# Kernel optimization log

Measured on AMD Instinct MI355X. Metric: run time of the kernel, lower is better.

Reference implementation:

```python
import jax, jax.numpy as jnp
import numpy as np

B, S, E, D, H, DH, FF, L = 8, 1024, 256, 1024, 16, 64, 4096, 12
TIME_DIM = 4096
MAX_PERIOD = 10000.0


def setup_inputs() -> dict:
    key = jax.random.key(0)
    ks = jax.random.split(key, 12)
    n = lambda k, shp: jax.random.normal(k, shp, dtype=jnp.float32) * 0.02
    return dict(
        inputs=jax.random.normal(ks[0], (B, S, 2 * E), dtype=jnp.float32),
        time=jax.random.uniform(ks[1], (B,), dtype=jnp.float32),
        in_W=n(ks[2], (2 * E, D)), in_b=jnp.zeros((D,), jnp.float32),
        out_W=n(ks[3], (D, E)), out_b=jnp.zeros((E,), jnp.float32),
        t_W1=n(ks[4], (D, TIME_DIM)), t_b1=jnp.zeros((TIME_DIM,), jnp.float32),
        t_W2=n(ks[5], (TIME_DIM, D)), t_b2=jnp.zeros((D,), jnp.float32),
        ln_scale=jnp.ones((L, D), jnp.float32),
        ln_bias=jnp.zeros((L, D), jnp.float32),
        proj_W=n(ks[6], (L, D, 3 * H * DH + 2 * FF)),
        attn_W=n(ks[7], (L, H * DH, D)),
        ff_W=n(ks[8], (L, FF, D)),
    )


def _layernorm(x, g, b):
    m = jnp.mean(x, axis=-1, keepdims=True)
    v = jnp.mean(jnp.square(x - m), axis=-1, keepdims=True)
    return (x - m) * jax.lax.rsqrt(v + 1e-5) * g + b


def reference(inputs, time, in_W, in_b, out_W, out_b, t_W1, t_b1, t_W2, t_b2,
              ln_scale, ln_bias, proj_W, attn_W, ff_W):
    # --- time embedding (SinusoidalTimeEmbedding -> Linear -> GELU -> Linear -> GELU) ---
    half = D // 2
    inv_ts = jnp.exp(jnp.arange(half, dtype=jnp.float32) * (-np.log(MAX_PERIOD) / (half - 1.0)))
    ts = time[:, None] * inv_ts[None, :]                      # [B, D/2]
    temb = jnp.concatenate([jnp.sin(ts), jnp.cos(ts)], -1)     # [B, D]
    temb = jax.nn.gelu(temb @ t_W1 + t_b1, approximate=False)
    temb = jax.nn.gelu(temb @ t_W2 + t_b2, approximate=False)  # [B, D]
    # --- fixed position embedding ---
    inv_freq = 1.0 / (MAX_PERIOD ** (jnp.arange(0, D, 2, dtype=jnp.float32) / D))
    sinu = jnp.arange(S, dtype=jnp.float32)[:, None] * inv_freq[None, :]  # [S, D/2]
    pos = jnp.concatenate([jnp.sin(sinu), jnp.cos(sinu)], -1)             # [S, D]
    # --- input projection + additive embeddings ---
    h = inputs @ in_W + in_b + pos[None] + temb[:, None, :]    # [B, S, D]
    scale = 1.0 / np.sqrt(DH)

    def block(h, params):
        g, bln, Wp, Wa, Wf = params
        u = _layernorm(h, g, bln)
        proj = u @ Wp                                          # [B, S, 3*H*DH + 2*FF]
        q, k, v, ff, gate = jnp.split(
            proj, [H * DH, 2 * H * DH, 3 * H * DH, 3 * H * DH + FF], axis=-1)
        q = q.reshape(B, S, H, DH).transpose(0, 2, 1, 3)       # [B, H, S, DH]
        k = k.reshape(B, S, H, DH).transpose(0, 2, 1, 3)
        v = v.reshape(B, S, H, DH).transpose(0, 2, 1, 3)
        score = jnp.einsum('bhsd,bhtd->bhst', q, k) * scale
        w = jax.nn.softmax(score, axis=-1)
        a = jnp.einsum('bhst,bhtd->bhsd', w, v)
        a = a.transpose(0, 2, 1, 3).reshape(B, S, H * DH)      # merge heads
        attn_out = a @ Wa
        ff_out = (ff * jax.nn.gelu(gate, approximate=True)) @ Wf  # tanh GELU per torch
        return h + attn_out + ff_out, None

    h, _ = jax.lax.scan(block, h, (ln_scale, ln_bias, proj_W, attn_W, ff_W))
    return h @ out_W + out_b
```

## Files before the change

kernel.cpp:

```cpp
#include <hip/hip_runtime.h>
#include <hip/hip_bf16.h>
#include <math.h>

static constexpr int B_ = 8, S_ = 1024, E_ = 256, D_ = 1024, H_ = 16, DH_ = 64,
                     FF_ = 4096, L_ = 12, TDIM_ = 4096;
static constexpr int BS_ = B_ * S_;
static constexpr int PROJN_ = 3 * H_ * DH_ + 2 * FF_;
static constexpr int PROJK_ = 2 * H_ * DH_;
static constexpr int AOW_ = H_ * DH_ + FF_;

typedef __attribute__((ext_vector_type(8))) short bf16x8;
typedef __attribute__((ext_vector_type(4))) short bf16x4;
typedef __attribute__((ext_vector_type(4))) float f32x4;

__device__ __forceinline__ float b2f(short b) {
    return __uint_as_float(((unsigned)(unsigned short)b) << 16);
}
__device__ __forceinline__ short f2b(float f) {
    __hip_bfloat16 h = __float2bfloat16(f);
    return *reinterpret_cast<short*>(&h);
}
__device__ __forceinline__ float gelu_exact(float x) {
    return 0.5f * x * (1.f + erff(x * 0.70710678118654752440f));
}
__device__ __forceinline__ float gelu_tanh(float x) {
    float u2 = 1.59576912160573070f * (x + 0.044715f * x * x * x);
    return x / (1.f + __expf(-u2));
}

#define GLOAD16(g, l)                                                     \
    __builtin_amdgcn_global_load_lds(                                     \
        (const __attribute__((address_space(1))) void*)(g),               \
        (__attribute__((address_space(3))) void*)(l), 16, 0, 0)

__global__ void temb0_kernel(const float* __restrict__ time, float* __restrict__ temb0) {
    int b = blockIdx.x;
    int i = threadIdx.x;
    float inv_ts = expf((float)i * (-logf(10000.f) / 511.f));
    float ts = time[b] * inv_ts;
    temb0[b * D_ + i] = sinf(ts);
    temb0[b * D_ + 512 + i] = cosf(ts);
}

__global__ void pos_kernel(float* __restrict__ pos) {
    int s = blockIdx.x;
    int j = threadIdx.x;
    float inv_freq = expf((float)j * (-logf(10000.f) / 512.f));
    float arg = (float)s * inv_freq;
    pos[s * D_ + j] = sinf(arg);
    pos[s * D_ + 512 + j] = cosf(arg);
}

__global__ void tmlp_kernel(const float* __restrict__ A, const float* __restrict__ Bw,
                            const float* __restrict__ bias, float* __restrict__ C,
                            int K, int N) {
    __shared__ float Ast[8][256];
    __shared__ float red2[16][16][9];
    int t = threadIdx.x;
    int col = t & 15, ks = t >> 4;
    int n = blockIdx.x * 16 + col;
    float acc[8];
#pragma unroll
    for (int b = 0; b < 8; ++b) acc[b] = 0.f;
    for (int c0 = 0; c0 < K; c0 += 256) {
#pragma unroll
        for (int i = 0; i < 8; ++i) {
            int idx = t + i * 256;
            Ast[idx >> 8][idx & 255] = A[(idx >> 8) * K + c0 + (idx & 255)];
        }
        __syncthreads();
#pragma unroll
        for (int i = 0; i < 16; ++i) {
            int k = ks * 16 + i;
            float w = Bw[(size_t)(c0 + k) * N + n];
#pragma unroll
            for (int b = 0; b < 8; ++b) acc[b] = fmaf(Ast[b][k], w, acc[b]);
        }
        __syncthreads();
    }
#pragma unroll
    for (int b = 0; b < 8; ++b) red2[ks][col][b] = acc[b];
    __syncthreads();
    if (t < 128) {
        int c2 = t >> 3, b = t & 7;
        float s = 0.f;
#pragma unroll
        for (int k2 = 0; k2 < 16; ++k2) s += red2[k2][c2][b];
        int nn = blockIdx.x * 16 + c2;
        C[(size_t)b * N + nn] = gelu_exact(s + bias[nn]);
    }
}

__global__ void f2b4_kernel(const float* __restrict__ in, __hip_bfloat16* __restrict__ out) {
    size_t i = ((size_t)blockIdx.x * 256 + threadIdx.x) * 4;
    float4 v = *reinterpret_cast<const float4*>(in + i);
    bf16x4 o;
    o[0] = f2b(v.x); o[1] = f2b(v.y); o[2] = f2b(v.z); o[3] = f2b(v.w);
    *reinterpret_cast<bf16x4*>(reinterpret_cast<short*>(out) + i) = o;
}

__device__ __forceinline__ void convT_body(const float* __restrict__ W,
                                           __hip_bfloat16* __restrict__ Wt,
                                           int K, int N, int outStride, int colOff,
                                           int perm, int bx, int by) {
    __shared__ float tile[64][65];
    int t = threadIdx.x;
    int n0 = bx * 64, k0 = by * 64;
#pragma unroll
    for (int i = 0; i < 4; ++i) {
        int idx = t + i * 256;
        int row = idx >> 4, c4 = (idx & 15) * 4;
        float4 v = *reinterpret_cast<const float4*>(W + (size_t)(k0 + row) * N + n0 + c4);
        tile[row][c4 + 0] = v.x; tile[row][c4 + 1] = v.y;
        tile[row][c4 + 2] = v.z; tile[row][c4 + 3] = v.w;
    }
    __syncthreads();
#pragma unroll
    for (int i = 0; i < 4; ++i) {
        int idx = t + i * 256;
        int n = idx >> 4, k4 = (idx & 15) * 4;
        int ng = n0 + n;
        size_t orow;
        if (perm) {
            if (ng < 3072) orow = ng;
            else if (ng < 7168) { int j = ng - 3072; orow = 3072 + (j >> 7) * 256 + (j & 127); }
            else { int j = ng - 7168; orow = 3072 + (j >> 7) * 256 + 128 + (j & 127); }
        } else {
            orow = ng;
        }
        bf16x4 o;
#pragma unroll
        for (int j = 0; j < 4; ++j) o[j] = f2b(tile[k4 + j][n]);
        *reinterpret_cast<bf16x4*>(reinterpret_cast<short*>(Wt) + orow * outStride + colOff + k0 + k4) = o;
    }
}

__global__ void convT_kernel(const float* __restrict__ W, __hip_bfloat16* __restrict__ Wt,
                             int K, int N, int outStride, int colOff) {
    convT_body(W, Wt, K, N, outStride, colOff, 0, blockIdx.x, blockIdx.y);
}

__global__ void convT3_kernel(const float* __restrict__ Wp, const float* __restrict__ Wa,
                              const float* __restrict__ Wf, __hip_bfloat16* __restrict__ Wpt,
                              __hip_bfloat16* __restrict__ Waft) {
    int bid = blockIdx.x;
    if (bid < 2816) {
        convT_body(Wp, Wpt, D_, PROJN_, D_, 0, 1, bid % 176, bid / 176);
    } else if (bid < 3072) {
        int i2 = bid - 2816;
        convT_body(Wa, Waft, D_, D_, AOW_, 0, 0, i2 & 15, i2 >> 4);
    } else {
        int i2 = bid - 3072;
        convT_body(Wf, Waft, FF_, D_, AOW_, D_, 0, i2 & 15, i2 >> 4);
    }
}

__global__ void ln_kernel(const float* __restrict__ h, const float* __restrict__ g,
                          const float* __restrict__ bb, __hip_bfloat16* __restrict__ u) {
    int row = blockIdx.x;
    int t = threadIdx.x;
    const float4 v = reinterpret_cast<const float4*>(h + (size_t)row * D_)[t];
    __shared__ float red[8];
    float s = v.x + v.y + v.z + v.w;
    for (int m8 = 1; m8 < 64; m8 <<= 1) s += __shfl_xor(s, m8, 64);
    if ((t & 63) == 0) red[t >> 6] = s;
    __syncthreads();
    float mean = (red[0] + red[1] + red[2] + red[3]) * (1.f / 1024.f);
    float dx = v.x - mean, dy = v.y - mean, dz = v.z - mean, dw = v.w - mean;
    float sq = dx * dx + dy * dy + dz * dz + dw * dw;
    for (int m8 = 1; m8 < 64; m8 <<= 1) sq += __shfl_xor(sq, m8, 64);
    if ((t & 63) == 0) red[4 + (t >> 6)] = sq;
    __syncthreads();
    float var = (red[4] + red[5] + red[6] + red[7]) * (1.f / 1024.f);
    float inv = rsqrtf(var + 1e-5f);
    int c = t * 4;
    bf16x4 o;
    o[0] = f2b(dx * inv * g[c + 0] + bb[c + 0]);
    o[1] = f2b(dy * inv * g[c + 1] + bb[c + 1]);
    o[2] = f2b(dz * inv * g[c + 2] + bb[c + 2]);
    o[3] = f2b(dw * inv * g[c + 3] + bb[c + 3]);
    *reinterpret_cast<bf16x4*>(reinterpret_cast<short*>(u) + (size_t)row * D_ + c) = o;
}

template <int MODE, int BIAS, int ADDPE>
__global__ __launch_bounds__(256) void mfma_gemm(
    const __hip_bfloat16* __restrict__ A, const __hip_bfloat16* __restrict__ Bt,
    const float* __restrict__ bias, float* __restrict__ Cf,
    __hip_bfloat16* __restrict__ Cb, const float* __restrict__ pe_pos,
    const float* __restrict__ pe_temb, int M, int N, int K) {
    __shared__ __align__(16) char As[128 * 64];
    __shared__ __align__(16) char Bs[128 * 64];
    int t = threadIdx.x;
    int lane = t & 63, wid = t >> 6;
    int m0 = blockIdx.y * 128, n0 = blockIdx.x * 128;
    size_t rowb = (size_t)K * 2;
    int srow = wid * 32 + (lane >> 2);
    int scol = (lane & 3) * 16;
    const char* ag0 = (const char*)A + (size_t)(m0 + srow) * rowb + scol;
    const char* ag1 = (const char*)A + (size_t)(m0 + srow + 16) * rowb + scol;
    const char* bg0 = (const char*)Bt + (size_t)(n0 + srow) * rowb + scol;
    const char* bg1 = (const char*)Bt + (size_t)(n0 + srow + 16) * rowb + scol;
    int lb0 = wid * 32 * 64;
    int lb1 = lb0 + 16 * 64;
    int wr = (wid >> 1) * 64, wc = (wid & 1) * 64;
    int lr = lane & 15;
    int a_base = (wr + lr) * 64 + (lane >> 4) * 16;
    int b_base = (wc + lr) * 64 + (lane >> 4) * 16;
    f32x4 acc[4][4] = {};
    int nkt = K >> 5;
    for (int kt = 0; kt < nkt; ++kt) {
        GLOAD16(ag0, As + lb0);
        GLOAD16(ag1, As + lb1);
        GLOAD16(bg0, Bs + lb0);
        GLOAD16(bg1, Bs + lb1);
        ag0 += 64; ag1 += 64; bg0 += 64; bg1 += 64;
        __syncthreads();
        bf16x8 af[4], bf[4];
#pragma unroll
        for (int f = 0; f < 4; ++f) {
            af[f] = *reinterpret_cast<const bf16x8*>(As + a_base + f * 1024);
            bf[f] = *reinterpret_cast<const bf16x8*>(Bs + b_base + f * 1024);
        }
        __builtin_amdgcn_s_setprio(1);
#pragma unroll
        for (int i = 0; i < 4; ++i)
#pragma unroll
            for (int j = 0; j < 4; ++j)
                acc[i][j] = __builtin_amdgcn_mfma_f32_16x16x32_bf16(af[i], bf[j], acc[i][j], 0, 0, 0);
        __builtin_amdgcn_s_setprio(0);
        __syncthreads();
    }
    int crow0 = m0 + wr + (lane >> 4) * 4;
    int ccol0 = n0 + wc + lr;
#pragma unroll
    for (int i = 0; i < 4; ++i) {
#pragma unroll
        for (int j = 0; j < 4; ++j) {
            int col = ccol0 + j * 16;
            float bv = BIAS ? bias[col] : 0.f;
            f32x4 v = acc[i][j];
#pragma unroll
            for (int r = 0; r < 4; ++r) {
                int row = crow0 + i * 16 + r;
                size_t o = (size_t)row * N + col;
                float val = v[r] + bv;
                if (ADDPE)
                    val += pe_pos[(size_t)(row & 1023) * D_ + col] +
                           pe_temb[(size_t)(row >> 10) * D_ + col];
                if (MODE == 0) Cf[o] = val;
                else if (MODE == 1) Cb[o] = __float2bfloat16(val);
                else Cf[o] += val;
            }
        }
    }
}

template <int MODE>
__global__ __launch_bounds__(512, 2) void gemm256(
    const __hip_bfloat16* __restrict__ A, const __hip_bfloat16* __restrict__ Bt,
    float* __restrict__ Cf, __hip_bfloat16* __restrict__ Cb,
    __hip_bfloat16* __restrict__ Fb, __hip_bfloat16* __restrict__ Vt,
    int M, int N, int K) {
    __shared__ __align__(16) char lds[131072];
    const int t = threadIdx.x;
    const int lane = t & 63, wid = t >> 6;
    const int lr = lane & 15, g = lane >> 4;
    const int wr = wid >> 2, wc = wid & 3;
    const int nbx = gridDim.x;
    const int nwg = nbx * gridDim.y;
    const int bid = blockIdx.y * nbx + blockIdx.x;
    const int swz = (bid & 7) * (nwg >> 3) + (bid >> 3);
    const int bx = swz % nbx, by = swz / nbx;
    const int m0 = by * 256, n0 = bx * 256;
    const size_t rowb = (size_t)K * 2;
    const int NT = K >> 6;
    const int srow = lane >> 2;
    const int scol = ((lane & 3) ^ (((lane >> 5) & 1) << 1)) * 16;
    const int ga = (g ^ (((lr >> 3) & 1) << 1)) * 16;
    const int arow = wr * 16 + lr;
    const int brow = wc * 16 + lr;
    const char* Ab = (const char*)A;
    const char* Bb = (const char*)Bt;

    auto stage = [&](int mat, int kt, int hh) {
        if (kt >= NT) return;
        int rbase = (mat ? n0 : m0) + hh * 128 + wid * 16 + srow;
        const char* src = (mat ? Bb : Ab) + (size_t)rbase * rowb + (size_t)kt * 128 + scol;
        char* dst = lds + mat * 65536 + (kt & 1) * 32768 + (hh * 128 + wid * 16) * 64;
        GLOAD16(src, dst);
        GLOAD16(src + 64, dst + 16384);
    };

    f32x4 acc[8][4] = {};
    bf16x8 af[4][2], bfr[4][2];

    stage(0, 0, 0); stage(0, 0, 1); stage(1, 0, 0); stage(1, 0, 1);
    stage(0, 1, 0); stage(1, 1, 0); stage(1, 1, 1);
    asm volatile("s_waitcnt vmcnt(6)" ::: "memory");
    __builtin_amdgcn_s_barrier();

    for (int kt = 0; kt < NT; ++kt) {
        const int p = kt & 1;
        const char* la = lds + p * 32768;
        const char* lb = lds + 65536 + p * 32768;
#pragma unroll
        for (int mi = 0; mi < 4; ++mi)
#pragma unroll
            for (int kk = 0; kk < 2; ++kk)
                af[mi][kk] = *reinterpret_cast<const bf16x8*>(
                    la + kk * 16384 + (mi * 32 + arow) * 64 + ga);
#pragma unroll
        for (int n = 0; n < 2; ++n)
#pragma unroll
            for (int kk = 0; kk < 2; ++kk)
                bfr[n][kk] = *reinterpret_cast<const bf16x8*>(
                    lb + kk * 16384 + (n * 64 + brow) * 64 + ga);
        stage(0, kt + 1, 1);
        __builtin_amdgcn_s_barrier();
        asm volatile("s_waitcnt lgkmcnt(0)" ::: "memory");
        __builtin_amdgcn_sched_barrier(0);
        __builtin_amdgcn_s_setprio(1);
#pragma unroll
        for (int mi = 0; mi < 4; ++mi)
#pragma unroll
            for (int n = 0; n < 2; ++n)
#pragma unroll
                for (int kk = 0; kk < 2; ++kk)
                    acc[mi][n] = __builtin_amdgcn_mfma_f32_16x16x32_bf16(
                        af[mi][kk], bfr[n][kk], acc[mi][n], 0, 0, 0);
        __builtin_amdgcn_s_setprio(0);
        __builtin_amdgcn_s_barrier();
#pragma unroll
        for (int n = 2; n < 4; ++n)
#pragma unroll
            for (int kk = 0; kk < 2; ++kk)
                bfr[n][kk] = *reinterpret_cast<const bf16x8*>(
                    lb + kk * 16384 + (n * 64 + brow) * 64 + ga);
        stage(0, kt + 2, 0);
        __builtin_amdgcn_s_barrier();
        asm volatile("s_waitcnt lgkmcnt(0)" ::: "memory");
        __builtin_amdgcn_sched_barrier(0);
        __builtin_amdgcn_s_setprio(1);
#pragma unroll
        for (int mi = 0; mi < 4; ++mi)
#pragma unroll
            for (int n = 2; n < 4; ++n)
#pragma unroll
                for (int kk = 0; kk < 2; ++kk)
                    acc[mi][n] = __builtin_amdgcn_mfma_f32_16x16x32_bf16(
                        af[mi][kk], bfr[n][kk], acc[mi][n], 0, 0, 0);
        __builtin_amdgcn_s_setprio(0);
        __builtin_amdgcn_s_barrier();
#pragma unroll
        for (int mi = 0; mi < 4; ++mi)
#pragma unroll
            for (int kk = 0; kk < 2; ++kk)
                af[mi][kk] = *reinterpret_cast<const bf16x8*>(
                    la + kk * 16384 + ((mi + 4) * 32 + arow) * 64 + ga);
        stage(1, kt + 2, 0);
        __builtin_amdgcn_s_barrier();
        asm volatile("s_waitcnt lgkmcnt(0)" ::: "memory");
        __builtin_amdgcn_sched_barrier(0);
        __builtin_amdgcn_s_setprio(1);
#pragma unroll
        for (int mi = 0; mi < 4; ++mi)
#pragma unroll
            for (int n = 2; n < 4; ++n)
#pragma unroll
                for (int kk = 0; kk < 2; ++kk)
                    acc[mi + 4][n] = __builtin_amdgcn_mfma_f32_16x16x32_bf16(
                        af[mi][kk], bfr[n][kk], acc[mi + 4][n], 0, 0, 0);
        __builtin_amdgcn_s_setprio(0);
        __builtin_amdgcn_s_barrier();
        stage(1, kt + 2, 1);
        if (kt < NT - 2) {
            asm volatile("s_waitcnt vmcnt(6)" ::: "memory");
        } else {
            asm volatile("s_waitcnt vmcnt(0)" ::: "memory");
        }
        __builtin_amdgcn_s_barrier();
        __builtin_amdgcn_s_setprio(1);
#pragma unroll
        for (int mi = 0; mi < 4; ++mi)
#pragma unroll
            for (int n = 0; n < 2; ++n)
#pragma unroll
                for (int kk = 0; kk < 2; ++kk)
                    acc[mi + 4][n] = __builtin_amdgcn_mfma_f32_16x16x32_bf16(
                        af[mi][kk], bfr[n][kk], acc[mi + 4][n], 0, 0, 0);
        __builtin_amdgcn_s_setprio(0);
        __builtin_amdgcn_s_barrier();
    }
    if (MODE == 3 && bx >= 12) {
        int jb = (bx - 12) * 128;
#pragma unroll
        for (int m = 0; m < 8; ++m) {
            int crow = m0 + m * 32 + wr * 16 + g * 4;
#pragma unroll
            for (int n = 0; n < 2; ++n) {
                int ffcol = jb + n * 64 + wc * 16 + lr;
                f32x4 fv = acc[m][n];
                f32x4 gv = acc[m][n + 2];
#pragma unroll
                for (int r = 0; r < 4; ++r) {
                    float val = fv[r] * gelu_tanh(gv[r]);
                    Fb[(size_t)(crow + r) * AOW_ + ffcol] = __float2bfloat16(val);
                }
            }
        }
        return;
    }
    if (MODE == 3 && bx >= 8) {
#pragma unroll
        for (int m = 0; m < 8; ++m) {
            int crow = m0 + m * 32 + wr * 16 + g * 4;
            int b = crow >> 10, s = crow & 1023;
#pragma unroll
            for (int n = 0; n < 4; ++n) {
                int col = n0 + n * 64 + wc * 16 + lr;
                int head = (col - 2048) >> 6, d = col & 63;
                f32x4 v = acc[m][n];
                bf16x4 o;
#pragma unroll
                for (int r = 0; r < 4; ++r) o[r] = f2b(v[r]);
                *reinterpret_cast<bf16x4*>(
                    reinterpret_cast<short*>(Vt) +
                    ((size_t)(b * 16 + head) * 64 + d) * 1024 + s) = o;
            }
        }
        return;
    }
#pragma unroll
    for (int m = 0; m < 8; ++m) {
        int crow = m0 + m * 32 + wr * 16 + g * 4;
#pragma unroll
        for (int n = 0; n < 4; ++n) {
            int col = n0 + n * 64 + wc * 16 + lr;
            f32x4 v = acc[m][n];
#pragma unroll
            for (int r = 0; r < 4; ++r) {
                if (MODE == 3) Cb[(size_t)(crow + r) * PROJK_ + col] = __float2bfloat16(v[r]);
                else if (MODE == 0) Cf[(size_t)(crow + r) * N + col] = v[r];
                else if (MODE == 1) Cb[(size_t)(crow + r) * N + col] = __float2bfloat16(v[r]);
                else Cf[(size_t)(crow + r) * N + col] += v[r];
            }
        }
    }
}

__global__ __launch_bounds__(256, 2) void attn_kernel(
    const __hip_bfloat16* __restrict__ proj, const __hip_bfloat16* __restrict__ vt,
    __hip_bfloat16* __restrict__ ao) {
    __shared__ __align__(16) char ksm[64 * 128];
    __shared__ __align__(16) char vsm[64 * 128];
    __shared__ __align__(16) char psm[4 * 16 * 128];
    int wgid = blockIdx.x;
    int xcd = wgid & 7, slot = wgid >> 3;
    int group = xcd * 16 + (slot >> 4);
    int qt = slot & 15;
    int head = group & 15, b = group >> 4;
    int t = threadIdx.x;
    int lane = t & 63, w = t >> 6;
    int r = lane & 15, g = lane >> 4;
    int r7s = (r & 7) << 4;
    int q0 = qt * 64;
    int qcol = head * 64;
    const __hip_bfloat16* pb = proj + (size_t)b * S_ * PROJK_;
    const char* vtb = (const char*)(vt + ((size_t)(b * 16 + head) * 64) * 1024);
    bf16x8 qf[2];
#pragma unroll
    for (int kk = 0; kk < 2; ++kk)
        qf[kk] = *reinterpret_cast<const bf16x8*>(
            pb + (size_t)(q0 + w * 16 + r) * PROJK_ + qcol + kk * 32 + g * 8);
    int srow8 = lane >> 3;
    int sgrp = lane & 7;
    float m = -1e30f, l = 0.f;
    f32x4 o_acc[4] = {};
    char* pw = psm + w * 2048;
    for (int kt = 0; kt < 16; ++kt) {
        int k0 = kt * 64;
#pragma unroll
        for (int c = 0; c < 2; ++c) {
            int krow = w * 16 + c * 8 + srow8;
            const __hip_bfloat16* src =
                pb + (size_t)(k0 + krow) * PROJK_ + 1024 + qcol + ((sgrp ^ (krow & 7)) << 3);
            GLOAD16(src, ksm + (w * 16 + c * 8) * 128);
        }
#pragma unroll
        for (int c = 0; c < 2; ++c) {
            int drow = w * 16 + c * 8 + srow8;
            const char* src = vtb + (size_t)drow * 2048 + k0 * 2 + ((sgrp ^ (drow & 7)) << 4);
            GLOAD16(src, vsm + (w * 16 + c * 8) * 128);
        }
        __syncthreads();
        f32x4 st[4] = {};
        __builtin_amdgcn_s_setprio(1);
#pragma unroll
        for (int j = 0; j < 4; ++j) {
#pragma unroll
            for (int kk = 0; kk < 2; ++kk) {
                bf16x8 kf = *reinterpret_cast<const bf16x8*>(
                    ksm + (j * 16 + r) * 128 + ((((kk * 4 + g) << 4) ^ r7s)));
                st[j] = __builtin_amdgcn_mfma_f32_16x16x32_bf16(kf, qf[kk], st[j], 0, 0, 0);
            }
        }
        __builtin_amdgcn_s_setprio(0);
        float tmax = -1e30f;
#pragma unroll
        for (int j = 0; j < 4; ++j)
#pragma unroll
            for (int rr = 0; rr < 4; ++rr) {
                st[j][rr] *= 0.125f;
                tmax = fmaxf(tmax, st[j][rr]);
            }
        tmax = fmaxf(tmax, __shfl_xor(tmax, 16, 64));
        tmax = fmaxf(tmax, __shfl_xor(tmax, 32, 64));
        float mnew = fmaxf(m, tmax);
        float rsum = 0.f;
#pragma unroll
        for (int j = 0; j < 4; ++j)
#pragma unroll
            for (int rr = 0; rr < 4; ++rr) {
                float p = __expf(st[j][rr] - mnew);
                st[j][rr] = p;
                rsum += p;
            }
        rsum += __shfl_xor(rsum, 16, 64);
        rsum += __shfl_xor(rsum, 32, 64);
        float alpha = __expf(m - mnew);
        l = l * alpha + rsum;
        m = mnew;
#pragma unroll
        for (int j = 0; j < 4; ++j)
#pragma unroll
            for (int rr = 0; rr < 4; ++rr) {
                int kv2 = j * 32 + g * 8 + rr * 2;
                *reinterpret_cast<short*>(pw + r * 128 + (kv2 ^ r7s)) = f2b(st[j][rr]);
            }
        asm volatile("s_waitcnt lgkmcnt(0)" ::: "memory");
        __builtin_amdgcn_sched_barrier(0);
        float ar[4];
#pragma unroll
        for (int rr = 0; rr < 4; ++rr) ar[rr] = __shfl(alpha, g * 4 + rr, 64);
#pragma unroll
        for (int dt = 0; dt < 4; ++dt)
#pragma unroll
            for (int rr = 0; rr < 4; ++rr) o_acc[dt][rr] *= ar[rr];
        __builtin_amdgcn_s_setprio(1);
#pragma unroll
        for (int kk = 0; kk < 2; ++kk) {
            bf16x8 pf = *reinterpret_cast<const bf16x8*>(
                pw + r * 128 + ((((kk * 4 + g) << 4) ^ r7s)));
#pragma unroll
            for (int dt = 0; dt < 4; ++dt) {
                bf16x8 vf = *reinterpret_cast<const bf16x8*>(
                    vsm + (dt * 16 + r) * 128 + ((((kk * 4 + g) << 4) ^ r7s)));
                o_acc[dt] = __builtin_amdgcn_mfma_f32_16x16x32_bf16(pf, vf, o_acc[dt], 0, 0, 0);
            }
        }
        __builtin_amdgcn_s_setprio(0);
        __syncthreads();
    }
    float linv = 1.f / l;
    float lr4[4];
#pragma unroll
    for (int rr = 0; rr < 4; ++rr) lr4[rr] = __shfl(linv, g * 4 + rr, 64);
    short* ap = reinterpret_cast<short*>(ao);
#pragma unroll
    for (int dt = 0; dt < 4; ++dt)
#pragma unroll
        for (int rr = 0; rr < 4; ++rr) {
            size_t o = ((size_t)b * S_ + q0 + w * 16 + g * 4 + rr) * (size_t)AOW_ +
                       qcol + dt * 16 + r;
            ap[o] = f2b(o_acc[dt][rr] * lr4[rr]);
        }
}

extern "C" void kernel_launch(void* const* d_in, const int* in_sizes, int n_in,
                              void* d_out, int out_size, void* d_ws, size_t ws_size,
                              hipStream_t stream) {
    const float* inputs = (const float*)d_in[0];
    const float* time = (const float*)d_in[1];
    const float* in_W = (const float*)d_in[2];
    const float* in_b = (const float*)d_in[3];
    const float* out_W = (const float*)d_in[4];
    const float* out_b = (const float*)d_in[5];
    const float* t_W1 = (const float*)d_in[6];
    const float* t_b1 = (const float*)d_in[7];
    const float* t_W2 = (const float*)d_in[8];
    const float* t_b2 = (const float*)d_in[9];
    const float* ln_scale = (const float*)d_in[10];
    const float* ln_bias = (const float*)d_in[11];
    const float* proj_W = (const float*)d_in[12];
    const float* attn_W = (const float*)d_in[13];
    const float* ff_W = (const float*)d_in[14];
    float* out = (float*)d_out;

    float* ws = (float*)d_ws;
    size_t off = 0;
    float* temb0 = ws + off; off += 8 * 1024;
    float* tact = ws + off;  off += 8 * 4096;
    float* temb = ws + off;  off += 8 * 1024;
    float* pos = ws + off;   off += (size_t)S_ * D_;
    float* h = ws + off;     off += (size_t)BS_ * D_;
    __hip_bfloat16* u = (__hip_bfloat16*)(ws + off);      off += (size_t)BS_ * D_ / 2;
    __hip_bfloat16* proj = (__hip_bfloat16*)(ws + off);   off += (size_t)BS_ * PROJK_ / 2;
    __hip_bfloat16* vt = (__hip_bfloat16*)(ws + off);     off += (size_t)BS_ * D_ / 2;
    __hip_bfloat16* ao = (__hip_bfloat16*)(ws + off);     off += (size_t)BS_ * AOW_ / 2;
    __hip_bfloat16* hb = (__hip_bfloat16*)(ws + off);     off += (size_t)BS_ * D_ / 2;
    __hip_bfloat16* inbf = (__hip_bfloat16*)(ws + off);   off += (size_t)BS_ * (2 * E_) / 2;
    __hip_bfloat16* in_Wt = (__hip_bfloat16*)(ws + off);  off += (size_t)(2 * E_) * D_ / 2;
    __hip_bfloat16* out_Wt = (__hip_bfloat16*)(ws + off); off += (size_t)D_ * E_ / 2;
    __hip_bfloat16* Wpt = (__hip_bfloat16*)(ws + off);    off += (size_t)D_ * PROJN_ / 2;
    __hip_bfloat16* Waft = (__hip_bfloat16*)(ws + off);   off += (size_t)D_ * AOW_ / 2;

    dim3 blk(256);

    temb0_kernel<<<B_, 512, 0, stream>>>(time, temb0);
    tmlp_kernel<<<TDIM_ / 16, blk, 0, stream>>>(temb0, t_W1, t_b1, tact, D_, TDIM_);
    tmlp_kernel<<<D_ / 16, blk, 0, stream>>>(tact, t_W2, t_b2, temb, TDIM_, D_);
    pos_kernel<<<S_, 512, 0, stream>>>(pos);
    f2b4_kernel<<<(BS_ * 2 * E_) / 1024, blk, 0, stream>>>(inputs, inbf);
    convT_kernel<<<dim3(D_ / 64, (2 * E_) / 64), blk, 0, stream>>>(
        in_W, in_Wt, 2 * E_, D_, 2 * E_, 0);
    convT_kernel<<<dim3(E_ / 64, D_ / 64), blk, 0, stream>>>(
        out_W, out_Wt, D_, E_, D_, 0);
    mfma_gemm<0, 1, 1><<<dim3(D_ / 128, BS_ / 128), blk, 0, stream>>>(
        inbf, in_Wt, in_b, h, nullptr, pos, temb, BS_, D_, 2 * E_);

    for (int l = 0; l < L_; ++l) {
        const float* Wp = proj_W + (size_t)l * D_ * PROJN_;
        const float* Wa = attn_W + (size_t)l * (H_ * DH_) * D_;
        const float* Wf = ff_W + (size_t)l * FF_ * D_;
        convT3_kernel<<<dim3(4096), blk, 0, stream>>>(Wp, Wa, Wf, Wpt, Waft);
        ln_kernel<<<BS_, blk, 0, stream>>>(h, ln_scale + l * D_, ln_bias + l * D_, u);
        gemm256<3><<<dim3(PROJN_ / 256, BS_ / 256), dim3(512), 0, stream>>>(
            u, Wpt, nullptr, proj, ao + D_, vt, BS_, PROJN_, D_);
        attn_kernel<<<dim3(2048), blk, 0, stream>>>(proj, vt, ao);
        mfma_gemm<2, 0, 0><<<dim3(D_ / 128, BS_ / 128), blk, 0, stream>>>(
            ao, Waft, nullptr, h, nullptr, nullptr, nullptr, BS_, D_, AOW_);
    }
    f2b4_kernel<<<(BS_ * D_) / 1024, blk, 0, stream>>>(h, hb);
    mfma_gemm<0, 1, 0><<<dim3(E_ / 128, BS_ / 128), blk, 0, stream>>>(
        hb, out_Wt, out_b, out, nullptr, nullptr, nullptr, BS_, E_, D_);
}
```

Baseline: 5.392 ms.

## Replace output GEMM with 256x128 pipelined MFMA kernel, fuse final bf16 cast

```diff
diff --git a/kernel.cpp b/kernel.cpp
--- a/kernel.cpp
+++ b/kernel.cpp
@@ -448,6 +448,161 @@
     }
 }
 
+template <int EMITB>
+__global__ __launch_bounds__(512, 1) void gemm256b(
+    const __hip_bfloat16* __restrict__ A, const __hip_bfloat16* __restrict__ Bt,
+    float* __restrict__ Cf, __hip_bfloat16* __restrict__ Cb, int M, int N, int K) {
+    __shared__ __align__(16) char lds[98304];
+    const int t = threadIdx.x;
+    const int lane = t & 63, wid = t >> 6;
+    const int lr = lane & 15, g = lane >> 4;
+    const int wr = wid >> 1, wc = wid & 1;
+    const int nbx = gridDim.x;
+    const int nwg = nbx * gridDim.y;
+    const int bid = blockIdx.y * nbx + blockIdx.x;
+    const int swz = (bid & 7) * (nwg >> 3) + (bid >> 3);
+    const int bx = swz % nbx, by = swz / nbx;
+    const int m0 = by * 256, n0 = bx * 128;
+    const size_t rowb = (size_t)K * 2;
+    const int NT = K >> 6;
+    const int srow = lane >> 2;
+    const int scol = ((lane & 3) ^ (((lane >> 5) & 1) << 1)) * 16;
+    const int ga = (g ^ (((lr >> 3) & 1) << 1)) * 16;
+
+    auto stageA = [&](int kt, int hh) {
+        if (kt >= NT) return;
+        int rowg = hh * 128 + wid * 16 + srow;
+        const char* src = (const char*)A + (size_t)(m0 + rowg) * rowb + (size_t)kt * 128 + scol;
+        char* dst = lds + (kt & 1) * 32768 + (hh * 128 + wid * 16) * 64;
+        GLOAD16(src, dst);
+        GLOAD16(src + 64, dst + 16384);
+    };
+    auto stageB = [&](int kt) {
+        if (kt >= NT) return;
+        int rowg = wid * 16 + srow;
+        const char* src = (const char*)Bt + (size_t)(n0 + rowg) * rowb + (size_t)kt * 128 + scol;
+        char* dst = lds + 65536 + (kt & 1) * 16384 + (wid * 16) * 64;
+        GLOAD16(src, dst);
+        GLOAD16(src + 64, dst + 8192);
+    };
+
+    f32x4 acc[4][4] = {};
+    bf16x8 af[2][2], bfr[4][2];
+
+    stageA(0, 0); stageA(0, 1); stageB(0);
+    stageA(1, 0); stageB(1);
+    asm volatile("s_waitcnt vmcnt(4)" ::: "memory");
+    __builtin_amdgcn_s_barrier();
+
+    for (int kt = 0; kt < NT; ++kt) {
+        const int p = kt & 1;
+        const char* la = lds + p * 32768;
+        const char* lb = lds + 65536 + p * 16384;
+#pragma unroll
+        for (int mi = 0; mi < 2; ++mi)
+#pragma unroll
+            for (int kk = 0; kk < 2; ++kk)
+                af[mi][kk] = *reinterpret_cast<const bf16x8*>(
+                    la + kk * 16384 + (mi * 64 + wr * 16 + lr) * 64 + ga);
+#pragma unroll
+        for (int n = 0; n < 2; ++n)
+#pragma unroll
+            for (int kk = 0; kk < 2; ++kk)
+                bfr[n][kk] = *reinterpret_cast<const bf16x8*>(
+                    lb + kk * 8192 + (wc * 64 + n * 16 + lr) * 64 + ga);
+        stageA(kt + 1, 1);
+        __builtin_amdgcn_s_barrier();
+        asm volatile("s_waitcnt lgkmcnt(0)" ::: "memory");
+        __builtin_amdgcn_sched_barrier(0);
+        __builtin_amdgcn_s_setprio(1);
+#pragma unroll
+        for (int mi = 0; mi < 2; ++mi)
+#pragma unroll
+            for (int n = 0; n < 2; ++n)
+#pragma unroll
+                for (int kk = 0; kk < 2; ++kk)
+                    acc[mi][n] = __builtin_amdgcn_mfma_f32_16x16x32_bf16(
+                        af[mi][kk], bfr[n][kk], acc[mi][n], 0, 0, 0);
+        __builtin_amdgcn_s_setprio(0);
+        __builtin_amdgcn_s_barrier();
+#pragma unroll
+        for (int n = 2; n < 4; ++n)
+#pragma unroll
+            for (int kk = 0; kk < 2; ++kk)
+                bfr[n][kk] = *reinterpret_cast<const bf16x8*>(
+                    lb + kk * 8192 + (wc * 64 + n * 16 + lr) * 64 + ga);
+        stageA(kt + 2, 0);
+        __builtin_amdgcn_s_barrier();
+        asm volatile("s_waitcnt lgkmcnt(0)" ::: "memory");
+        __builtin_amdgcn_sched_barrier(0);
+        __builtin_amdgcn_s_setprio(1);
+#pragma unroll
+        for (int mi = 0; mi < 2; ++mi)
+#pragma unroll
+            for (int n = 2; n < 4; ++n)
+#pragma unroll
+                for (int kk = 0; kk < 2; ++kk)
+                    acc[mi][n] = __builtin_amdgcn_mfma_f32_16x16x32_bf16(
+                        af[mi][kk], bfr[n][kk], acc[mi][n], 0, 0, 0);
+        __builtin_amdgcn_s_setprio(0);
+        __builtin_amdgcn_s_barrier();
+#pragma unroll
+        for (int mi = 0; mi < 2; ++mi)
+#pragma unroll
+            for (int kk = 0; kk < 2; ++kk)
+                af[mi][kk] = *reinterpret_cast<const bf16x8*>(
+                    la + kk * 16384 + ((mi + 2) * 64 + wr * 16 + lr) * 64 + ga);
+        stageB(kt + 2);
+        __builtin_amdgcn_s_barrier();
+        asm volatile("s_waitcnt lgkmcnt(0)" ::: "memory");
+        __builtin_amdgcn_sched_barrier(0);
+        __builtin_amdgcn_s_setprio(1);
+#pragma unroll
+        for (int mi = 0; mi < 2; ++mi)
+#pragma unroll
+            for (int n = 2; n < 4; ++n)
+#pragma unroll
+                for (int kk = 0; kk < 2; ++kk)
+                    acc[mi + 2][n] = __builtin_amdgcn_mfma_f32_16x16x32_bf16(
+                        af[mi][kk], bfr[n][kk], acc[mi + 2][n], 0, 0, 0);
+        __builtin_amdgcn_s_setprio(0);
+        __builtin_amdgcn_s_barrier();
+        if (kt < NT - 2) {
+            asm volatile("s_waitcnt vmcnt(4)" ::: "memory");
+        } else {
+            asm volatile("s_waitcnt vmcnt(0)" ::: "memory");
+        }
+        __builtin_amdgcn_s_barrier();
+        __builtin_amdgcn_s_setprio(1);
+#pragma unroll
+        for (int mi = 0; mi < 2; ++mi)
+#pragma unroll
+            for (int n = 0; n < 2; ++n)
+#pragma unroll
+                for (int kk = 0; kk < 2; ++kk)
+                    acc[mi + 2][n] = __builtin_amdgcn_mfma_f32_16x16x32_bf16(
+                        af[mi][kk], bfr[n][kk], acc[mi + 2][n], 0, 0, 0);
+        __builtin_amdgcn_s_setprio(0);
+        __builtin_amdgcn_s_barrier();
+    }
+#pragma unroll
+    for (int mq = 0; mq < 4; ++mq) {
+        int crow = m0 + mq * 64 + wr * 16 + g * 4;
+#pragma unroll
+        for (int nq = 0; nq < 4; ++nq) {
+            int col = n0 + wc * 64 + nq * 16 + lr;
+            f32x4 v = acc[mq][nq];
+#pragma unroll
+            for (int r = 0; r < 4; ++r) {
+                size_t o = (size_t)(crow + r) * N + col;
+                float nv = Cf[o] + v[r];
+                Cf[o] = nv;
+                if (EMITB) Cb[o] = __float2bfloat16(nv);
+            }
+        }
+    }
+}
+
 __global__ __launch_bounds__(256, 2) void attn_kernel(
     const __hip_bfloat16* __restrict__ proj, const __hip_bfloat16* __restrict__ vt,
     __hip_bfloat16* __restrict__ ao) {
@@ -637,10 +792,13 @@
         gemm256<3><<<dim3(PROJN_ / 256, BS_ / 256), dim3(512), 0, stream>>>(
             u, Wpt, nullptr, proj, ao + D_, vt, BS_, PROJN_, D_);
         attn_kernel<<<dim3(2048), blk, 0, stream>>>(proj, vt, ao);
-        mfma_gemm<2, 0, 0><<<dim3(D_ / 128, BS_ / 128), blk, 0, stream>>>(
-            ao, Waft, nullptr, h, nullptr, nullptr, nullptr, BS_, D_, AOW_);
-    }
-    f2b4_kernel<<<(BS_ * D_) / 1024, blk, 0, stream>>>(h, hb);
+        if (l == L_ - 1)
+            gemm256b<1><<<dim3(D_ / 128, BS_ / 256), dim3(512), 0, stream>>>(
+                ao, Waft, h, hb, BS_, D_, AOW_);
+        else
+            gemm256b<0><<<dim3(D_ / 128, BS_ / 256), dim3(512), 0, stream>>>(
+                ao, Waft, h, nullptr, BS_, D_, AOW_);
+    }
     mfma_gemm<0, 1, 0><<<dim3(E_ / 128, BS_ / 128), blk, 0, stream>>>(
         hb, out_Wt, out_b, out, nullptr, nullptr, nullptr, BS_, E_, D_);
 }
```

New measurement: 4.891 ms. 1.1x faster.
